# Kernel tuning notes

Hardware: AMD Instinct MI355X
Metric: run time of the kernel (lower is better)

Reference implementation:

```python
import jax, jax.numpy as jnp
import numpy as np

N = 100000          # nodes
E = 1600000         # edges (avg degree 16)
DIN = 64
DOUT = 64
EXPERTS = 3
GATE_C = 4
TEMP = 101.0        # batch=0 < decay_lim: 100 - 0 + final_temperature(1.0)


def setup_inputs() -> dict:
    key = jax.random.key(0)
    ks = jax.random.split(key, 6)
    x = jax.random.normal(ks[0], (N, DIN), dtype=jnp.float32)
    edge_index = jax.random.randint(ks[1], (2, E), 0, N, dtype=jnp.int32)
    gate_features = jax.random.normal(ks[2], (N, GATE_C), dtype=jnp.float32)
    # per-expert GCN linear weights/bias (PyG GCNConv: lin then bias)
    W = jax.random.normal(ks[3], (EXPERTS, DIN, DOUT), dtype=jnp.float32) / np.sqrt(DIN).astype(np.float32)
    b = jnp.zeros((EXPERTS, DOUT), dtype=jnp.float32)
    # gating nn.Linear(gate_channels, experts, bias=False); stored as [GATE_C, EXPERTS] so y = gf @ Wg
    Wg = jax.random.normal(ks[4], (GATE_C, EXPERTS), dtype=jnp.float32) / np.sqrt(GATE_C).astype(np.float32)
    return {"x": x, "edge_index": edge_index, "gate_features": gate_features,
            "W": W, "b": b, "Wg": Wg}


def reference(x, edge_index, gate_features, W, b, Wg):
    n = x.shape[0]
    # --- GCN normalization with self-loops (PyG GCNConv defaults) ---
    loops = jnp.arange(n, dtype=edge_index.dtype)
    rows = jnp.concatenate([edge_index[0], loops])   # source nodes, [E+N]
    cols = jnp.concatenate([edge_index[1], loops])   # target nodes, [E+N]
    deg = jax.ops.segment_sum(jnp.ones(rows.shape, dtype=x.dtype), cols, num_segments=n)
    dinv = jnp.where(deg > 0, jax.lax.rsqrt(deg), 0.0)
    norm = dinv[rows] * dinv[cols]                   # [E+N]

    # --- gating network (softmax with decayed temperature) ---
    gate = jax.nn.softmax((gate_features @ Wg) / jnp.asarray(TEMP, x.dtype), axis=-1)  # [N, EXPERTS]

    # --- experts: GCN conv -> ReLU -> gate-weighted accumulation ---
    out = jnp.zeros((n, W.shape[-1]), dtype=x.dtype)
    for i in range(W.shape[0]):                      # small fixed expert count
        xw = x @ W[i]                                # [N, DOUT]
        msg = xw[rows] * norm[:, None]               # gather + scale, [E+N, DOUT]
        agg = jax.ops.segment_sum(msg, cols, num_segments=n) + b[i]
        out = out + gate[:, i:i + 1] * jax.nn.relu(agg)
    return out
```

## Files before the change

kernel.cpp:

```cpp
#include <hip/hip_runtime.h>
#include <hip/hip_bf16.h>

#define NN 100000
#define NE 1600000
#define NT 6250

#define NBUCK  511
#define BRANGE 196
#define CAPB   3584
#define CHUNK  2048
#define NCH    782

typedef __attribute__((ext_vector_type(8))) short bf16x8;
typedef __attribute__((ext_vector_type(4))) float f32x4;

__device__ inline float2 bf16x2_unpack(unsigned v) {
    float2 r;
    r.x = __uint_as_float(v << 16);
    r.y = __uint_as_float(v & 0xffff0000u);
    return r;
}
__device__ inline unsigned bf16x2_pack(float a, float b) {
    __hip_bfloat162 h2(__float2bfloat16(a), __float2bfloat16(b));
    unsigned u;
    __builtin_memcpy(&u, &h2, 4);
    return u;
}

__global__ __launch_bounds__(256) void bin_kernel(const int* __restrict__ rows,
                                                  const int* __restrict__ cols,
                                                  int* __restrict__ cur,
                                                  unsigned* __restrict__ eb) {
    __shared__ int hist[512];
    __shared__ int excl[512];
    __shared__ int lcur[512];
    __shared__ int gbase[512];
    __shared__ int s2[256];
    __shared__ unsigned staged[CHUNK];
    __shared__ unsigned short bktarr[CHUNK];
    int t = threadIdx.x;
    int base = blockIdx.x * CHUNK;
    int cnt = min(CHUNK, NE - base);

    hist[t] = 0; hist[t + 256] = 0;
    __syncthreads();
    #pragma unroll
    for (int k = 0; k < CHUNK / 256; k++) {
        int i = k * 256 + t;
        if (i < cnt) {
            int c = cols[base + i];
            atomicAdd(&hist[(unsigned)c / BRANGE], 1);
        }
    }
    __syncthreads();
    int a0 = hist[2 * t], a1 = hist[2 * t + 1];
    s2[t] = a0 + a1;
    __syncthreads();
    #pragma unroll
    for (int off = 1; off < 256; off <<= 1) {
        int v = (t >= off) ? s2[t - off] : 0;
        __syncthreads();
        s2[t] += v;
        __syncthreads();
    }
    int pe = (t > 0) ? s2[t - 1] : 0;
    excl[2 * t] = pe;      excl[2 * t + 1] = pe + a0;
    lcur[2 * t] = pe;      lcur[2 * t + 1] = pe + a0;
    gbase[2 * t]     = a0 ? atomicAdd(cur + 2 * t, a0) : 0;
    gbase[2 * t + 1] = a1 ? atomicAdd(cur + 2 * t + 1, a1) : 0;
    __syncthreads();
    #pragma unroll
    for (int k = 0; k < CHUNK / 256; k++) {
        int i = k * 256 + t;
        if (i < cnt) {
            int c = cols[base + i];
            int r = rows[base + i];
            int bkt = (unsigned)c / BRANGE;
            int lp = atomicAdd(&lcur[bkt], 1);
            staged[lp] = ((unsigned)(c - bkt * BRANGE) << 24) | (unsigned)r;
            bktarr[lp] = (unsigned short)bkt;
        }
    }
    __syncthreads();
    #pragma unroll
    for (int k = 0; k < CHUNK / 256; k++) {
        int i = k * 256 + t;
        if (i < cnt) {
            int bkt = bktarr[i];
            int pos = gbase[bkt] + (i - excl[bkt]);
            if (pos < CAPB) eb[(size_t)bkt * CAPB + pos] = staged[i];
        }
    }
}

__global__ __launch_bounds__(512) void nodesort_kernel(const int* __restrict__ cur,
                                                       const unsigned* __restrict__ eb,
                                                       int* __restrict__ srcs2,
                                                       int2* __restrict__ nsd) {
    __shared__ int hist[256];
    __shared__ int sx[256];
    __shared__ int lcur[BRANGE];
    int b = blockIdx.x, t = threadIdx.x;
    if (t < 256) hist[t] = 0;
    __syncthreads();
    int cnt = min(cur[b], CAPB);
    const unsigned* seg = eb + (size_t)b * CAPB;
    for (int e = t; e < cnt; e += 512) atomicAdd(&hist[seg[e] >> 24], 1);
    __syncthreads();
    if (t < 256) sx[t] = hist[t];
    __syncthreads();
    #pragma unroll
    for (int off = 1; off < 256; off <<= 1) {
        int v = (t < 256 && t >= off) ? sx[t - off] : 0;
        __syncthreads();
        if (t < 256) sx[t] += v;
        __syncthreads();
    }
    if (t < BRANGE) {
        int ex = (t > 0) ? sx[t - 1] : 0;
        lcur[t] = ex;
        int n = b * BRANGE + t;
        if (n < NN) nsd[n] = make_int2(ex, hist[t]);
    }
    __syncthreads();
    for (int e = t; e < cnt; e += 512) {
        unsigned rec = seg[e];
        int p = atomicAdd(&lcur[rec >> 24], 1);
        srcs2[(size_t)b * CAPB + p] = rec & 0xFFFFFFu;
    }
}

__global__ __launch_bounds__(256) void xscale_kernel(const float* __restrict__ x,
                                                     const int2* __restrict__ nsd,
                                                     unsigned* __restrict__ xs) {
    int i = blockIdx.x * 256 + threadIdx.x;
    int n = i >> 5;
    int d = (i & 31) * 2;
    float2 v = *(const float2*)(x + (size_t)n * 64 + d);
    float dv = rsqrtf((float)(nsd[n].y + 1));
    xs[i] = bf16x2_pack(v.x * dv, v.y * dv);
}

__global__ __launch_bounds__(256) void gather_kernel(const int* __restrict__ srcs2,
                                                     const int2* __restrict__ nsd,
                                                     const unsigned* __restrict__ xs,
                                                     unsigned* __restrict__ hbu) {
    int lane = threadIdx.x & 63;
    int wave = threadIdx.x >> 6;
    int g  = lane >> 4;
    int gl = lane & 15;
    int gb = g << 4;

    int n = blockIdx.x * 16 + wave * 4 + g;
    int2 sd = nsd[n];
    int deg = sd.y;
    int bkt = (unsigned)n / BRANGE;
    const int* seg = srcs2 + (size_t)bkt * CAPB + sd.x;
    const uint2* xsv = (const uint2*)xs;

    float4 acc = make_float4(0.f, 0.f, 0.f, 0.f);
    for (int base = 0; base < deg; base += 16) {
        int idx = 0;
        if (base + gl < deg) idx = seg[base + gl];
        int s0 = __shfl(idx, gb);
        #pragma unroll
        for (int c = 0; c < 16; c += 8) {
            uint2 v[8];
            #pragma unroll
            for (int j = 0; j < 8; j++) {
                int s = __shfl(idx, gb + c + j);
                s = (base + c + j < deg) ? s : s0;
                v[j] = xsv[(size_t)s * 16 + gl];
            }
            #pragma unroll
            for (int j = 0; j < 8; j++) {
                if (base + c + j < deg) {
                    float2 f0 = bf16x2_unpack(v[j].x);
                    float2 f1 = bf16x2_unpack(v[j].y);
                    acc.x += f0.x; acc.y += f0.y;
                    acc.z += f1.x; acc.w += f1.y;
                }
            }
        }
    }
    uint2 svu = xsv[(size_t)n * 16 + gl];
    float2 sv0 = bf16x2_unpack(svu.x);
    float2 sv1 = bf16x2_unpack(svu.y);
    float dn = rsqrtf((float)(deg + 1));
    uint2 o;
    o.x = bf16x2_pack((acc.x + sv0.x) * dn, (acc.y + sv0.y) * dn);
    o.y = bf16x2_pack((acc.z + sv1.x) * dn, (acc.w + sv1.y) * dn);
    ((uint2*)hbu)[(size_t)n * 16 + gl] = o;
}

__global__ void wpack_kernel(const float* __restrict__ W, __hip_bfloat16* __restrict__ Bp) {
    int idx = blockIdx.x * 256 + threadIdx.x;
    if (idx >= 12288) return;
    int j    = idx & 7;
    int lane = (idx >> 3) & 63;
    int rest = idx >> 9;
    int t    = rest % 12;
    int kh   = rest / 12;
    int k    = kh * 32 + (lane >> 4) * 8 + j;
    int col  = t * 16 + (lane & 15);
    int i    = col >> 6;
    int d    = col & 63;
    Bp[idx] = __float2bfloat16(W[(i * 64 + k) * 64 + d]);
}

__global__ __launch_bounds__(256) void mfma_kernel(const __hip_bfloat16* __restrict__ hb,
                                                   const short* __restrict__ Bp,
                                                   const float* __restrict__ b,
                                                   const float* __restrict__ gf,
                                                   const float* __restrict__ Wg,
                                                   float* __restrict__ out) {
    int wave = threadIdx.x >> 6;
    int lane = threadIdx.x & 63;
    int tile = blockIdx.x * 4 + wave;
    if (tile >= NT) return;
    int n0 = tile * 16;
    int m = lane & 15, quad = lane >> 4;

    const short* hrow = (const short*)hb + ((size_t)(n0 + m)) * 64 + quad * 8;
    bf16x8 a0 = *(const bf16x8*)(hrow);
    bf16x8 a1 = *(const bf16x8*)(hrow + 32);

    f32x4 acc[12];
    #pragma unroll
    for (int t = 0; t < 12; t++) acc[t] = (f32x4)(0.0f);

    #pragma unroll
    for (int kh = 0; kh < 2; kh++) {
        bf16x8 a = kh ? a1 : a0;
        #pragma unroll
        for (int t = 0; t < 12; t++) {
            bf16x8 bf = *(const bf16x8*)(Bp + ((size_t)((kh * 12 + t) * 64 + lane)) * 8);
            acc[t] = __builtin_amdgcn_mfma_f32_16x16x32_bf16(a, bf, acc[t], 0, 0, 0);
        }
    }

    float wg[12];
    #pragma unroll
    for (int k = 0; k < 12; k++) wg[k] = Wg[k];

    #pragma unroll
    for (int reg = 0; reg < 4; reg++) {
        int n = n0 + quad * 4 + reg;
        float4 g = ((const float4*)gf)[n];
        float l0 = (g.x*wg[0] + g.y*wg[3] + g.z*wg[6] + g.w*wg[9])  * (1.0f/101.0f);
        float l1 = (g.x*wg[1] + g.y*wg[4] + g.z*wg[7] + g.w*wg[10]) * (1.0f/101.0f);
        float l2 = (g.x*wg[2] + g.y*wg[5] + g.z*wg[8] + g.w*wg[11]) * (1.0f/101.0f);
        float mx = fmaxf(l0, fmaxf(l1, l2));
        float e0 = __expf(l0 - mx), e1 = __expf(l1 - mx), e2 = __expf(l2 - mx);
        float inv = 1.0f / (e0 + e1 + e2);
        float g0 = e0 * inv, g1 = e1 * inv, g2 = e2 * inv;
        #pragma unroll
        for (int dpos = 0; dpos < 4; dpos++) {
            int d = dpos * 16 + m;
            float v0 = acc[0*4 + dpos][reg] + b[0*64 + d];
            float v1 = acc[1*4 + dpos][reg] + b[1*64 + d];
            float v2 = acc[2*4 + dpos][reg] + b[2*64 + d];
            float o = g0 * fmaxf(v0, 0.f) + g1 * fmaxf(v1, 0.f) + g2 * fmaxf(v2, 0.f);
            out[(size_t)n * 64 + d] = o;
        }
    }
}

extern "C" void kernel_launch(void* const* d_in, const int* in_sizes, int n_in,
                              void* d_out, int out_size, void* d_ws, size_t ws_size,
                              hipStream_t stream) {
    const float* x  = (const float*)d_in[0];
    const int*   ei = (const int*)d_in[1];
    const float* gf = (const float*)d_in[2];
    const float* W  = (const float*)d_in[3];
    const float* b  = (const float*)d_in[4];
    const float* Wg = (const float*)d_in[5];
    float* out = (float*)d_out;
    const int* rows = ei;
    const int* cols = ei + NE;

    char* ws = (char*)d_ws;
    size_t off = 0;
    auto alloc = [&](size_t bytes) {
        char* p = ws + off;
        off = (off + bytes + 255) & ~(size_t)255;
        return p;
    };
    int*            cur    = (int*)alloc(512 * 4);
    unsigned*       eb     = (unsigned*)alloc((size_t)NBUCK * CAPB * 4);
    int*            srcs2  = (int*)alloc((size_t)NBUCK * CAPB * 4);
    int2*           nsd    = (int2*)alloc((size_t)NN * 8);
    unsigned*       xs     = (unsigned*)alloc((size_t)NN * 32 * 4);
    unsigned*       hbu    = (unsigned*)alloc((size_t)NN * 32 * 4);
    __hip_bfloat16* Bp     = (__hip_bfloat16*)alloc(12288 * 2);

    hipMemsetAsync(cur, 0, 512 * 4, stream);

    bin_kernel<<<NCH, 256, 0, stream>>>(rows, cols, cur, eb);
    nodesort_kernel<<<NBUCK, 512, 0, stream>>>(cur, eb, srcs2, nsd);
    xscale_kernel<<<NN * 32 / 256, 256, 0, stream>>>(x, nsd, xs);
    wpack_kernel<<<48, 256, 0, stream>>>(W, Bp);
    gather_kernel<<<NN / 16, 256, 0, stream>>>(srcs2, nsd, xs, hbu);
    mfma_kernel<<<(NT + 3) / 4, 256, 0, stream>>>((const __hip_bfloat16*)hbu,
                                                  (const short*)Bp, b, gf, Wg, out);
}
```

Measured before the change: 194.7 us.

## Replace two-level bucket sort CSR build with atomic degree count and scatter

Replaces the bucketed binning plus per-bucket node sort with a simpler CSR construction: global atomic degree histogram, block-scan allocation of per-node segments via a global atomic counter, then per-edge atomic scatter of source indices. This removes the large staging buffers and the two shared-memory-heavy sort passes, but relies on global atomics with random addresses for both counting and scattering. Node segments are allocated in nondeterministic order, so the edge order within a node is nondeterministic and the source-index writes are uncoalesced.

```diff
diff --git a/kernel.cpp b/kernel.cpp
--- a/kernel.cpp
+++ b/kernel.cpp
@@ -4,12 +4,6 @@
 #define NN 100000
 #define NE 1600000
 #define NT 6250
-
-#define NBUCK  511
-#define BRANGE 196
-#define CAPB   3584
-#define CHUNK  2048
-#define NCH    782
 
 typedef __attribute__((ext_vector_type(8))) short bf16x8;
 typedef __attribute__((ext_vector_type(4))) float f32x4;
@@ -27,107 +21,61 @@
     return u;
 }
 
-__global__ __launch_bounds__(256) void bin_kernel(const int* __restrict__ rows,
-                                                  const int* __restrict__ cols,
-                                                  int* __restrict__ cur,
-                                                  unsigned* __restrict__ eb) {
-    __shared__ int hist[512];
-    __shared__ int excl[512];
-    __shared__ int lcur[512];
-    __shared__ int gbase[512];
-    __shared__ int s2[256];
-    __shared__ unsigned staged[CHUNK];
-    __shared__ unsigned short bktarr[CHUNK];
+__global__ __launch_bounds__(256) void deg_kernel(const int* __restrict__ cols,
+                                                  int* __restrict__ deg) {
+    int i = blockIdx.x * 1024 + threadIdx.x;
+    #pragma unroll
+    for (int k = 0; k < 4; k++) {
+        int e = i + k * 256;
+        if (e < NE) atomicAdd(&deg[cols[e]], 1);
+    }
+}
+
+__global__ __launch_bounds__(256) void alloc_kernel(const int* __restrict__ deg,
+                                                    int* __restrict__ galloc,
+                                                    int* __restrict__ nextpos,
+                                                    int2* __restrict__ nsd) {
+    __shared__ int wsum[4];
+    __shared__ int bbase;
     int t = threadIdx.x;
-    int base = blockIdx.x * CHUNK;
-    int cnt = min(CHUNK, NE - base);
-
-    hist[t] = 0; hist[t + 256] = 0;
+    int n = blockIdx.x * 256 + t;
+    int d = (n < NN) ? deg[n] : 0;
+    int lane = t & 63;
+    int wv = t >> 6;
+    int incl = d;
+    #pragma unroll
+    for (int off = 1; off < 64; off <<= 1) {
+        int v = __shfl_up(incl, off);
+        if (lane >= off) incl += v;
+    }
+    if (lane == 63) wsum[wv] = incl;
     __syncthreads();
-    #pragma unroll
-    for (int k = 0; k < CHUNK / 256; k++) {
-        int i = k * 256 + t;
-        if (i < cnt) {
-            int c = cols[base + i];
-            atomicAdd(&hist[(unsigned)c / BRANGE], 1);
-        }
+    if (t == 0) {
+        int s0 = wsum[0], s1 = wsum[1], s2 = wsum[2], s3 = wsum[3];
+        bbase = atomicAdd(galloc, s0 + s1 + s2 + s3);
+        wsum[0] = 0; wsum[1] = s0; wsum[2] = s0 + s1; wsum[3] = s0 + s1 + s2;
     }
     __syncthreads();
-    int a0 = hist[2 * t], a1 = hist[2 * t + 1];
-    s2[t] = a0 + a1;
-    __syncthreads();
-    #pragma unroll
-    for (int off = 1; off < 256; off <<= 1) {
-        int v = (t >= off) ? s2[t - off] : 0;
-        __syncthreads();
-        s2[t] += v;
-        __syncthreads();
-    }
-    int pe = (t > 0) ? s2[t - 1] : 0;
-    excl[2 * t] = pe;      excl[2 * t + 1] = pe + a0;
-    lcur[2 * t] = pe;      lcur[2 * t + 1] = pe + a0;
-    gbase[2 * t]     = a0 ? atomicAdd(cur + 2 * t, a0) : 0;
-    gbase[2 * t + 1] = a1 ? atomicAdd(cur + 2 * t + 1, a1) : 0;
-    __syncthreads();
-    #pragma unroll
-    for (int k = 0; k < CHUNK / 256; k++) {
-        int i = k * 256 + t;
-        if (i < cnt) {
-            int c = cols[base + i];
-            int r = rows[base + i];
-            int bkt = (unsigned)c / BRANGE;
-            int lp = atomicAdd(&lcur[bkt], 1);
-            staged[lp] = ((unsigned)(c - bkt * BRANGE) << 24) | (unsigned)r;
-            bktarr[lp] = (unsigned short)bkt;
-        }
-    }
-    __syncthreads();
-    #pragma unroll
-    for (int k = 0; k < CHUNK / 256; k++) {
-        int i = k * 256 + t;
-        if (i < cnt) {
-            int bkt = bktarr[i];
-            int pos = gbase[bkt] + (i - excl[bkt]);
-            if (pos < CAPB) eb[(size_t)bkt * CAPB + pos] = staged[i];
-        }
-    }
-}
-
-__global__ __launch_bounds__(512) void nodesort_kernel(const int* __restrict__ cur,
-                                                       const unsigned* __restrict__ eb,
-                                                       int* __restrict__ srcs2,
-                                                       int2* __restrict__ nsd) {
-    __shared__ int hist[256];
-    __shared__ int sx[256];
-    __shared__ int lcur[BRANGE];
-    int b = blockIdx.x, t = threadIdx.x;
-    if (t < 256) hist[t] = 0;
-    __syncthreads();
-    int cnt = min(cur[b], CAPB);
-    const unsigned* seg = eb + (size_t)b * CAPB;
-    for (int e = t; e < cnt; e += 512) atomicAdd(&hist[seg[e] >> 24], 1);
-    __syncthreads();
-    if (t < 256) sx[t] = hist[t];
-    __syncthreads();
-    #pragma unroll
-    for (int off = 1; off < 256; off <<= 1) {
-        int v = (t < 256 && t >= off) ? sx[t - off] : 0;
-        __syncthreads();
-        if (t < 256) sx[t] += v;
-        __syncthreads();
-    }
-    if (t < BRANGE) {
-        int ex = (t > 0) ? sx[t - 1] : 0;
-        lcur[t] = ex;
-        int n = b * BRANGE + t;
-        if (n < NN) nsd[n] = make_int2(ex, hist[t]);
-    }
-    __syncthreads();
-    for (int e = t; e < cnt; e += 512) {
-        unsigned rec = seg[e];
-        int p = atomicAdd(&lcur[rec >> 24], 1);
-        srcs2[(size_t)b * CAPB + p] = rec & 0xFFFFFFu;
-    }
+    int start = bbase + wsum[wv] + incl - d;
+    if (n < NN) {
+        nextpos[n] = start;
+        nsd[n] = make_int2(start, d);
+    }
+}
+
+__global__ __launch_bounds__(256) void scatter_kernel(const int* __restrict__ rows,
+                                                      const int* __restrict__ cols,
+                                                      int* __restrict__ nextpos,
+                                                      int* __restrict__ srcs) {
+    int i = blockIdx.x * 512 + threadIdx.x;
+    int c0 = cols[i];
+    int c1 = cols[i + 256];
+    int r0 = rows[i];
+    int r1 = rows[i + 256];
+    int p0 = atomicAdd(&nextpos[c0], 1);
+    int p1 = atomicAdd(&nextpos[c1], 1);
+    srcs[p0] = r0;
+    srcs[p1] = r1;
 }
 
 __global__ __launch_bounds__(256) void xscale_kernel(const float* __restrict__ x,
@@ -141,7 +89,7 @@
     xs[i] = bf16x2_pack(v.x * dv, v.y * dv);
 }
 
-__global__ __launch_bounds__(256) void gather_kernel(const int* __restrict__ srcs2,
+__global__ __launch_bounds__(256) void gather_kernel(const int* __restrict__ srcs,
                                                      const int2* __restrict__ nsd,
                                                      const unsigned* __restrict__ xs,
                                                      unsigned* __restrict__ hbu) {
@@ -154,8 +102,7 @@
     int n = blockIdx.x * 16 + wave * 4 + g;
     int2 sd = nsd[n];
     int deg = sd.y;
-    int bkt = (unsigned)n / BRANGE;
-    const int* seg = srcs2 + (size_t)bkt * CAPB + sd.x;
+    const int* seg = srcs + sd.x;
     const uint2* xsv = (const uint2*)xs;
 
     float4 acc = make_float4(0.f, 0.f, 0.f, 0.f);
@@ -286,21 +233,23 @@
         off = (off + bytes + 255) & ~(size_t)255;
         return p;
     };
-    int*            cur    = (int*)alloc(512 * 4);
-    unsigned*       eb     = (unsigned*)alloc((size_t)NBUCK * CAPB * 4);
-    int*            srcs2  = (int*)alloc((size_t)NBUCK * CAPB * 4);
-    int2*           nsd    = (int2*)alloc((size_t)NN * 8);
-    unsigned*       xs     = (unsigned*)alloc((size_t)NN * 32 * 4);
-    unsigned*       hbu    = (unsigned*)alloc((size_t)NN * 32 * 4);
-    __hip_bfloat16* Bp     = (__hip_bfloat16*)alloc(12288 * 2);
-
-    hipMemsetAsync(cur, 0, 512 * 4, stream);
-
-    bin_kernel<<<NCH, 256, 0, stream>>>(rows, cols, cur, eb);
-    nodesort_kernel<<<NBUCK, 512, 0, stream>>>(cur, eb, srcs2, nsd);
+    int*            galloc  = (int*)alloc(4);
+    int*            deg     = (int*)alloc((size_t)NN * 4);
+    int*            nextpos = (int*)alloc((size_t)NN * 4);
+    int*            srcs    = (int*)alloc((size_t)NE * 4);
+    int2*           nsd     = (int2*)alloc((size_t)NN * 8);
+    unsigned*       xs      = (unsigned*)alloc((size_t)NN * 32 * 4);
+    unsigned*       hbu     = (unsigned*)alloc((size_t)NN * 32 * 4);
+    __hip_bfloat16* Bp      = (__hip_bfloat16*)alloc(12288 * 2);
+
+    hipMemsetAsync(galloc, 0, 256 + (size_t)NN * 4, stream);
+
+    deg_kernel<<<(NE + 1023) / 1024, 256, 0, stream>>>(cols, deg);
+    alloc_kernel<<<(NN + 255) / 256, 256, 0, stream>>>(deg, galloc, nextpos, nsd);
     xscale_kernel<<<NN * 32 / 256, 256, 0, stream>>>(x, nsd, xs);
     wpack_kernel<<<48, 256, 0, stream>>>(W, Bp);
-    gather_kernel<<<NN / 16, 256, 0, stream>>>(srcs2, nsd, xs, hbu);
+    scatter_kernel<<<NE / 512, 256, 0, stream>>>(rows, cols, nextpos, srcs);
+    gather_kernel<<<NN / 16, 256, 0, stream>>>(srcs, nsd, xs, hbu);
     mfma_kernel<<<(NT + 3) / 4, 256, 0, stream>>>((const __hip_bfloat16*)hbu,
                                                   (const short*)Bp, b, gf, Wg, out);
 }
```

After: 335.1 us. +72.1%, slower.

## Replace per-node sort with bucket-level LDS atomic accumulation for aggregation

Applied to the files above, without the earlier changes.

Drops the second-level per-node sort (nodesort_kernel) and the staged coalesced write in binning. Edges are now scattered straight into coarse buckets, with global degree counting done by atomics. A new gacc kernel then gathers source features per bucket and accumulates them into a 196x64 float tile in LDS using shared-memory atomics, before applying self-loop and normalisation. This removes one kernel launch and one full pass over the edge arrays. In exchange it pays for global atomics on degree, uncoalesced bucket writes, and heavy LDS atomic contention, and it makes the float summation order nondeterministic. The cur counters are also padded to a stride of 16 to spread out global atomic contention.

```diff
diff --git a/kernel.cpp b/kernel.cpp
--- a/kernel.cpp
+++ b/kernel.cpp
@@ -27,17 +27,13 @@
     return u;
 }
 
-__global__ __launch_bounds__(256) void bin_kernel(const int* __restrict__ rows,
-                                                  const int* __restrict__ cols,
-                                                  int* __restrict__ cur,
-                                                  unsigned* __restrict__ eb) {
+__global__ __launch_bounds__(256) void bin2_kernel(const int* __restrict__ rows,
+                                                   const int* __restrict__ cols,
+                                                   int* __restrict__ cur,
+                                                   int* __restrict__ deg,
+                                                   unsigned* __restrict__ eb) {
     __shared__ int hist[512];
-    __shared__ int excl[512];
     __shared__ int lcur[512];
-    __shared__ int gbase[512];
-    __shared__ int s2[256];
-    __shared__ unsigned staged[CHUNK];
-    __shared__ unsigned short bktarr[CHUNK];
     int t = threadIdx.x;
     int base = blockIdx.x * CHUNK;
     int cnt = min(CHUNK, NE - base);
@@ -49,25 +45,16 @@
         int i = k * 256 + t;
         if (i < cnt) {
             int c = cols[base + i];
+            atomicAdd(&deg[c], 1);
             atomicAdd(&hist[(unsigned)c / BRANGE], 1);
         }
     }
     __syncthreads();
-    int a0 = hist[2 * t], a1 = hist[2 * t + 1];
-    s2[t] = a0 + a1;
-    __syncthreads();
-    #pragma unroll
-    for (int off = 1; off < 256; off <<= 1) {
-        int v = (t >= off) ? s2[t - off] : 0;
-        __syncthreads();
-        s2[t] += v;
-        __syncthreads();
-    }
-    int pe = (t > 0) ? s2[t - 1] : 0;
-    excl[2 * t] = pe;      excl[2 * t + 1] = pe + a0;
-    lcur[2 * t] = pe;      lcur[2 * t + 1] = pe + a0;
-    gbase[2 * t]     = a0 ? atomicAdd(cur + 2 * t, a0) : 0;
-    gbase[2 * t + 1] = a1 ? atomicAdd(cur + 2 * t + 1, a1) : 0;
+    #pragma unroll
+    for (int u = t; u < 512; u += 256) {
+        int h = hist[u];
+        lcur[u] = h ? atomicAdd(&cur[u * 16], h) : 0;
+    }
     __syncthreads();
     #pragma unroll
     for (int k = 0; k < CHUNK / 256; k++) {
@@ -76,121 +63,86 @@
             int c = cols[base + i];
             int r = rows[base + i];
             int bkt = (unsigned)c / BRANGE;
-            int lp = atomicAdd(&lcur[bkt], 1);
-            staged[lp] = ((unsigned)(c - bkt * BRANGE) << 24) | (unsigned)r;
-            bktarr[lp] = (unsigned short)bkt;
-        }
-    }
-    __syncthreads();
-    #pragma unroll
-    for (int k = 0; k < CHUNK / 256; k++) {
-        int i = k * 256 + t;
-        if (i < cnt) {
-            int bkt = bktarr[i];
-            int pos = gbase[bkt] + (i - excl[bkt]);
-            if (pos < CAPB) eb[(size_t)bkt * CAPB + pos] = staged[i];
-        }
-    }
-}
-
-__global__ __launch_bounds__(512) void nodesort_kernel(const int* __restrict__ cur,
-                                                       const unsigned* __restrict__ eb,
-                                                       int* __restrict__ srcs2,
-                                                       int2* __restrict__ nsd) {
-    __shared__ int hist[256];
-    __shared__ int sx[256];
-    __shared__ int lcur[BRANGE];
-    int b = blockIdx.x, t = threadIdx.x;
-    if (t < 256) hist[t] = 0;
-    __syncthreads();
-    int cnt = min(cur[b], CAPB);
-    const unsigned* seg = eb + (size_t)b * CAPB;
-    for (int e = t; e < cnt; e += 512) atomicAdd(&hist[seg[e] >> 24], 1);
-    __syncthreads();
-    if (t < 256) sx[t] = hist[t];
-    __syncthreads();
-    #pragma unroll
-    for (int off = 1; off < 256; off <<= 1) {
-        int v = (t < 256 && t >= off) ? sx[t - off] : 0;
-        __syncthreads();
-        if (t < 256) sx[t] += v;
-        __syncthreads();
-    }
-    if (t < BRANGE) {
-        int ex = (t > 0) ? sx[t - 1] : 0;
-        lcur[t] = ex;
-        int n = b * BRANGE + t;
-        if (n < NN) nsd[n] = make_int2(ex, hist[t]);
-    }
-    __syncthreads();
-    for (int e = t; e < cnt; e += 512) {
-        unsigned rec = seg[e];
-        int p = atomicAdd(&lcur[rec >> 24], 1);
-        srcs2[(size_t)b * CAPB + p] = rec & 0xFFFFFFu;
+            int p = atomicAdd(&lcur[bkt], 1);
+            if (p < CAPB)
+                eb[(size_t)bkt * CAPB + p] = ((unsigned)(c - bkt * BRANGE) << 24) | (unsigned)r;
+        }
     }
 }
 
 __global__ __launch_bounds__(256) void xscale_kernel(const float* __restrict__ x,
-                                                     const int2* __restrict__ nsd,
+                                                     const int* __restrict__ deg,
                                                      unsigned* __restrict__ xs) {
     int i = blockIdx.x * 256 + threadIdx.x;
     int n = i >> 5;
     int d = (i & 31) * 2;
     float2 v = *(const float2*)(x + (size_t)n * 64 + d);
-    float dv = rsqrtf((float)(nsd[n].y + 1));
+    float dv = rsqrtf((float)(deg[n] + 1));
     xs[i] = bf16x2_pack(v.x * dv, v.y * dv);
 }
 
-__global__ __launch_bounds__(256) void gather_kernel(const int* __restrict__ srcs2,
-                                                     const int2* __restrict__ nsd,
-                                                     const unsigned* __restrict__ xs,
-                                                     unsigned* __restrict__ hbu) {
-    int lane = threadIdx.x & 63;
-    int wave = threadIdx.x >> 6;
-    int g  = lane >> 4;
-    int gl = lane & 15;
-    int gb = g << 4;
-
-    int n = blockIdx.x * 16 + wave * 4 + g;
-    int2 sd = nsd[n];
-    int deg = sd.y;
-    int bkt = (unsigned)n / BRANGE;
-    const int* seg = srcs2 + (size_t)bkt * CAPB + sd.x;
-    const uint2* xsv = (const uint2*)xs;
-
-    float4 acc = make_float4(0.f, 0.f, 0.f, 0.f);
-    for (int base = 0; base < deg; base += 16) {
-        int idx = 0;
-        if (base + gl < deg) idx = seg[base + gl];
-        int s0 = __shfl(idx, gb);
+__global__ __launch_bounds__(512) void gacc_kernel(const int* __restrict__ cur,
+                                                   const unsigned* __restrict__ eb,
+                                                   const int* __restrict__ deg,
+                                                   const unsigned* __restrict__ xs,
+                                                   unsigned* __restrict__ hbu) {
+    __shared__ float acc[BRANGE * 64];
+    int b = blockIdx.x;
+    int t = threadIdx.x;
+    int lane = t & 63;
+    int wave = t >> 6;
+    int sub = lane >> 5;
+    int dp = lane & 31;
+
+    int cnt = min(cur[b * 16], CAPB);
+    const unsigned* seg = eb + (size_t)b * CAPB;
+
+    #pragma unroll
+    for (int i = t; i < BRANGE * 16; i += 512)
+        ((float4*)acc)[i] = make_float4(0.f, 0.f, 0.f, 0.f);
+    __syncthreads();
+
+    for (int wbase = wave * 64; wbase < cnt; wbase += 512) {
+        int nrec = min(64, cnt - wbase);
+        unsigned rec = (lane < nrec) ? seg[wbase + lane] : 0u;
+        unsigned rec0 = __shfl(rec, 0);
         #pragma unroll
-        for (int c = 0; c < 16; c += 8) {
-            uint2 v[8];
+        for (int c = 0; c < 64; c += 32) {
+            unsigned rr[16];
+            unsigned vb[16];
             #pragma unroll
-            for (int j = 0; j < 8; j++) {
-                int s = __shfl(idx, gb + c + j);
-                s = (base + c + j < deg) ? s : s0;
-                v[j] = xsv[(size_t)s * 16 + gl];
+            for (int j = 0; j < 16; j++) {
+                int k = c + 2 * j + sub;
+                unsigned s = __shfl(rec, k);
+                rr[j] = s;
+                unsigned sa = (k < nrec) ? s : rec0;
+                vb[j] = xs[(size_t)(sa & 0xFFFFFFu) * 32 + dp];
             }
             #pragma unroll
-            for (int j = 0; j < 8; j++) {
-                if (base + c + j < deg) {
-                    float2 f0 = bf16x2_unpack(v[j].x);
-                    float2 f1 = bf16x2_unpack(v[j].y);
-                    acc.x += f0.x; acc.y += f0.y;
-                    acc.z += f1.x; acc.w += f1.y;
+            for (int j = 0; j < 16; j++) {
+                int k = c + 2 * j + sub;
+                if (k < nrec) {
+                    float2 f = bf16x2_unpack(vb[j]);
+                    int local = rr[j] >> 24;
+                    atomicAdd(&acc[local * 64 + dp], f.x);
+                    atomicAdd(&acc[local * 64 + 32 + dp], f.y);
                 }
             }
         }
     }
-    uint2 svu = xsv[(size_t)n * 16 + gl];
-    float2 sv0 = bf16x2_unpack(svu.x);
-    float2 sv1 = bf16x2_unpack(svu.y);
-    float dn = rsqrtf((float)(deg + 1));
-    uint2 o;
-    o.x = bf16x2_pack((acc.x + sv0.x) * dn, (acc.y + sv0.y) * dn);
-    o.y = bf16x2_pack((acc.z + sv1.x) * dn, (acc.w + sv1.y) * dn);
-    ((uint2*)hbu)[(size_t)n * 16 + gl] = o;
+    __syncthreads();
+
+    int nloc = min(BRANGE, NN - b * BRANGE);
+    for (int i = t; i < nloc * 32; i += 512) {
+        int nl = i >> 5;
+        int d = i & 31;
+        int n = b * BRANGE + nl;
+        float2 f = bf16x2_unpack(xs[(size_t)n * 32 + d]);
+        float dn = rsqrtf((float)(deg[n] + 1));
+        float a0 = (acc[nl * 64 + d] + f.x) * dn;
+        float a1 = (acc[nl * 64 + 32 + d] + f.y) * dn;
+        hbu[(size_t)n * 32 + d] = bf16x2_pack(a0, a1);
+    }
 }
 
 __global__ void wpack_kernel(const float* __restrict__ W, __hip_bfloat16* __restrict__ Bp) {
@@ -286,21 +238,19 @@
         off = (off + bytes + 255) & ~(size_t)255;
         return p;
     };
-    int*            cur    = (int*)alloc(512 * 4);
-    unsigned*       eb     = (unsigned*)alloc((size_t)NBUCK * CAPB * 4);
-    int*            srcs2  = (int*)alloc((size_t)NBUCK * CAPB * 4);
-    int2*           nsd    = (int2*)alloc((size_t)NN * 8);
-    unsigned*       xs     = (unsigned*)alloc((size_t)NN * 32 * 4);
-    unsigned*       hbu    = (unsigned*)alloc((size_t)NN * 32 * 4);
-    __hip_bfloat16* Bp     = (__hip_bfloat16*)alloc(12288 * 2);
-
-    hipMemsetAsync(cur, 0, 512 * 4, stream);
-
-    bin_kernel<<<NCH, 256, 0, stream>>>(rows, cols, cur, eb);
-    nodesort_kernel<<<NBUCK, 512, 0, stream>>>(cur, eb, srcs2, nsd);
-    xscale_kernel<<<NN * 32 / 256, 256, 0, stream>>>(x, nsd, xs);
+    int*            cur = (int*)alloc(512 * 16 * 4);
+    int*            deg = (int*)alloc((size_t)NN * 4);
+    unsigned*       eb  = (unsigned*)alloc((size_t)NBUCK * CAPB * 4);
+    unsigned*       xs  = (unsigned*)alloc((size_t)NN * 32 * 4);
+    unsigned*       hbu = (unsigned*)alloc((size_t)NN * 32 * 4);
+    __hip_bfloat16* Bp  = (__hip_bfloat16*)alloc(12288 * 2);
+
+    hipMemsetAsync(cur, 0, 512 * 16 * 4 + (size_t)NN * 4, stream);
+
+    bin2_kernel<<<NCH, 256, 0, stream>>>(rows, cols, cur, deg, eb);
+    xscale_kernel<<<NN * 32 / 256, 256, 0, stream>>>(x, deg, xs);
     wpack_kernel<<<48, 256, 0, stream>>>(W, Bp);
-    gather_kernel<<<NN / 16, 256, 0, stream>>>(srcs2, nsd, xs, hbu);
+    gacc_kernel<<<NBUCK, 512, 0, stream>>>(cur, eb, deg, xs, hbu);
     mfma_kernel<<<(NT + 3) / 4, 256, 0, stream>>>((const __hip_bfloat16*)hbu,
                                                   (const short*)Bp, b, gf, Wg, out);
 }
```

Result: slower. 745.4 us (+282.9%).

## Pad bucket counters, stage node sort in LDS, widen gather batch

Applied to the files above, without the earlier changes.

Bucket counters are padded to 64-byte strides so the global atomics from different buckets no longer share cache lines. The per-bucket node sort now keeps records in shared memory, uses a wave-level shuffle scan instead of a barrier-heavy block scan, and writes sorted sources out coalesced rather than scattered. The gather loop issues 16 neighbour loads at once instead of two batches of 8, which raises memory-level parallelism at the cost of more registers. The larger static LDS footprint of the sort kernel may reduce its occupancy.

```diff
diff --git a/kernel.cpp b/kernel.cpp
--- a/kernel.cpp
+++ b/kernel.cpp
@@ -66,8 +66,8 @@
     int pe = (t > 0) ? s2[t - 1] : 0;
     excl[2 * t] = pe;      excl[2 * t + 1] = pe + a0;
     lcur[2 * t] = pe;      lcur[2 * t + 1] = pe + a0;
-    gbase[2 * t]     = a0 ? atomicAdd(cur + 2 * t, a0) : 0;
-    gbase[2 * t + 1] = a1 ? atomicAdd(cur + 2 * t + 1, a1) : 0;
+    gbase[2 * t]     = a0 ? atomicAdd(cur + 2 * t * 16, a0) : 0;
+    gbase[2 * t + 1] = a1 ? atomicAdd(cur + (2 * t + 1) * 16, a1) : 0;
     __syncthreads();
     #pragma unroll
     for (int k = 0; k < CHUNK / 256; k++) {
@@ -93,41 +93,53 @@
     }
 }
 
-__global__ __launch_bounds__(512) void nodesort_kernel(const int* __restrict__ cur,
-                                                       const unsigned* __restrict__ eb,
-                                                       int* __restrict__ srcs2,
-                                                       int2* __restrict__ nsd) {
+__global__ __launch_bounds__(512) void sortn_kernel(const int* __restrict__ cur,
+                                                    const unsigned* __restrict__ eb,
+                                                    int* __restrict__ srcs2,
+                                                    int2* __restrict__ nsd) {
+    __shared__ unsigned recs[CAPB];
+    __shared__ unsigned srcl[CAPB];
     __shared__ int hist[256];
-    __shared__ int sx[256];
-    __shared__ int lcur[BRANGE];
+    __shared__ int lcur[256];
     int b = blockIdx.x, t = threadIdx.x;
     if (t < 256) hist[t] = 0;
     __syncthreads();
-    int cnt = min(cur[b], CAPB);
+    int cnt = min(cur[b * 16], CAPB);
     const unsigned* seg = eb + (size_t)b * CAPB;
-    for (int e = t; e < cnt; e += 512) atomicAdd(&hist[seg[e] >> 24], 1);
-    __syncthreads();
-    if (t < 256) sx[t] = hist[t];
-    __syncthreads();
-    #pragma unroll
-    for (int off = 1; off < 256; off <<= 1) {
-        int v = (t < 256 && t >= off) ? sx[t - off] : 0;
-        __syncthreads();
-        if (t < 256) sx[t] += v;
-        __syncthreads();
-    }
-    if (t < BRANGE) {
-        int ex = (t > 0) ? sx[t - 1] : 0;
-        lcur[t] = ex;
-        int n = b * BRANGE + t;
-        if (n < NN) nsd[n] = make_int2(ex, hist[t]);
-    }
-    __syncthreads();
-    for (int e = t; e < cnt; e += 512) {
-        unsigned rec = seg[e];
-        int p = atomicAdd(&lcur[rec >> 24], 1);
-        srcs2[(size_t)b * CAPB + p] = rec & 0xFFFFFFu;
-    }
+    for (int i = t; i < cnt; i += 512) {
+        unsigned r = seg[i];
+        recs[i] = r;
+        atomicAdd(&hist[r >> 24], 1);
+    }
+    __syncthreads();
+    if (t < 64) {
+        int e = t * 4;
+        int h0 = hist[e], h1 = hist[e + 1], h2 = hist[e + 2], h3 = hist[e + 3];
+        int lsum = h0 + h1 + h2 + h3;
+        int inc = lsum;
+        #pragma unroll
+        for (int off = 1; off < 64; off <<= 1) {
+            int v = __shfl_up(inc, off);
+            if (t >= off) inc += v;
+        }
+        int ex = inc - lsum;
+        int e0 = ex, e1 = ex + h0, e2 = e1 + h1, e3 = e2 + h2;
+        lcur[e] = e0; lcur[e + 1] = e1; lcur[e + 2] = e2; lcur[e + 3] = e3;
+        int n = b * BRANGE + e;
+        if (e     < BRANGE && n     < NN) nsd[n]     = make_int2(e0, h0);
+        if (e + 1 < BRANGE && n + 1 < NN) nsd[n + 1] = make_int2(e1, h1);
+        if (e + 2 < BRANGE && n + 2 < NN) nsd[n + 2] = make_int2(e2, h2);
+        if (e + 3 < BRANGE && n + 3 < NN) nsd[n + 3] = make_int2(e3, h3);
+    }
+    __syncthreads();
+    for (int i = t; i < cnt; i += 512) {
+        unsigned r = recs[i];
+        int p = atomicAdd(&lcur[r >> 24], 1);
+        srcl[p] = r & 0xFFFFFFu;
+    }
+    __syncthreads();
+    for (int i = t; i < cnt; i += 512)
+        srcs2[(size_t)b * CAPB + i] = (int)srcl[i];
 }
 
 __global__ __launch_bounds__(256) void xscale_kernel(const float* __restrict__ x,
@@ -163,23 +175,20 @@
         int idx = 0;
         if (base + gl < deg) idx = seg[base + gl];
         int s0 = __shfl(idx, gb);
-        #pragma unroll
-        for (int c = 0; c < 16; c += 8) {
-            uint2 v[8];
-            #pragma unroll
-            for (int j = 0; j < 8; j++) {
-                int s = __shfl(idx, gb + c + j);
-                s = (base + c + j < deg) ? s : s0;
-                v[j] = xsv[(size_t)s * 16 + gl];
-            }
-            #pragma unroll
-            for (int j = 0; j < 8; j++) {
-                if (base + c + j < deg) {
-                    float2 f0 = bf16x2_unpack(v[j].x);
-                    float2 f1 = bf16x2_unpack(v[j].y);
-                    acc.x += f0.x; acc.y += f0.y;
-                    acc.z += f1.x; acc.w += f1.y;
-                }
+        uint2 v[16];
+        #pragma unroll
+        for (int j = 0; j < 16; j++) {
+            int s = __shfl(idx, gb + j);
+            s = (base + j < deg) ? s : s0;
+            v[j] = xsv[(size_t)s * 16 + gl];
+        }
+        #pragma unroll
+        for (int j = 0; j < 16; j++) {
+            if (base + j < deg) {
+                float2 f0 = bf16x2_unpack(v[j].x);
+                float2 f1 = bf16x2_unpack(v[j].y);
+                acc.x += f0.x; acc.y += f0.y;
+                acc.z += f1.x; acc.w += f1.y;
             }
         }
     }
@@ -286,18 +295,18 @@
         off = (off + bytes + 255) & ~(size_t)255;
         return p;
     };
-    int*            cur    = (int*)alloc(512 * 4);
-    unsigned*       eb     = (unsigned*)alloc((size_t)NBUCK * CAPB * 4);
-    int*            srcs2  = (int*)alloc((size_t)NBUCK * CAPB * 4);
-    int2*           nsd    = (int2*)alloc((size_t)NN * 8);
-    unsigned*       xs     = (unsigned*)alloc((size_t)NN * 32 * 4);
-    unsigned*       hbu    = (unsigned*)alloc((size_t)NN * 32 * 4);
-    __hip_bfloat16* Bp     = (__hip_bfloat16*)alloc(12288 * 2);
-
-    hipMemsetAsync(cur, 0, 512 * 4, stream);
+    int*            cur   = (int*)alloc(512 * 16 * 4);
+    unsigned*       eb    = (unsigned*)alloc((size_t)NBUCK * CAPB * 4);
+    int*            srcs2 = (int*)alloc((size_t)NBUCK * CAPB * 4);
+    int2*           nsd   = (int2*)alloc((size_t)NN * 8);
+    unsigned*       xs    = (unsigned*)alloc((size_t)NN * 32 * 4);
+    unsigned*       hbu   = (unsigned*)alloc((size_t)NN * 32 * 4);
+    __hip_bfloat16* Bp    = (__hip_bfloat16*)alloc(12288 * 2);
+
+    hipMemsetAsync(cur, 0, 512 * 16 * 4, stream);
 
     bin_kernel<<<NCH, 256, 0, stream>>>(rows, cols, cur, eb);
-    nodesort_kernel<<<NBUCK, 512, 0, stream>>>(cur, eb, srcs2, nsd);
+    sortn_kernel<<<NBUCK, 512, 0, stream>>>(cur, eb, srcs2, nsd);
     xscale_kernel<<<NN * 32 / 256, 256, 0, stream>>>(x, nsd, xs);
     wpack_kernel<<<48, 256, 0, stream>>>(W, Bp);
     gather_kernel<<<NN / 16, 256, 0, stream>>>(srcs2, nsd, xs, hbu);
```

After: 178.5 us. 1.09x faster.
